# Kernel optimization log

Measured on AMD Instinct MI355X. Metric: run time of the kernel, lower is better.

## Reference

```python
import jax, jax.numpy as jnp
import numpy as np

N_NODES = 100000
LAYER_NUM = 3


def gcn_conv(x, src, dst, W, b, n):
    # PyG GCNConv: add self-loops, symmetric normalization D^-1/2 (A+I) D^-1/2, x@W, +b
    h = x @ W                                   # [N, out]
    ones = jnp.ones(src.shape[0], dtype=h.dtype)
    deg = jax.ops.segment_sum(ones, dst, num_segments=n) + 1.0  # +1 for self-loop
    dinv = jax.lax.rsqrt(deg)                   # deg >= 1 always (self-loop)
    norm = dinv[src] * dinv[dst]                # [E]
    msgs = h[src] * norm[:, None]               # gather + scale, [E, out]
    agg = jax.ops.segment_sum(msgs, dst, num_segments=n)
    agg = agg + h * (dinv * dinv)[:, None]      # self-loop contribution
    return agg + b


def setup_inputs() -> dict:
    key = jax.random.key(0)
    ks = jax.random.split(key, 8)
    in_d, mid_d, out_d = 512, 256, 40
    n, e = N_NODES, 1600000
    x = jax.random.normal(ks[0], (n, in_d), dtype=jnp.float32)
    edge_index = jax.random.randint(ks[1], (2, e), 0, n, dtype=jnp.int64)
    def glorot(k, fan_in, fan_out):
        s = jnp.sqrt(6.0 / (fan_in + fan_out))
        return jax.random.uniform(k, (fan_in, fan_out), jnp.float32, -s, s)
    W1 = glorot(ks[2], in_d, mid_d)
    b1 = jnp.zeros((mid_d,), jnp.float32)
    Wi = glorot(ks[3], mid_d, mid_d)
    bi = jnp.zeros((mid_d,), jnp.float32)
    W2 = glorot(ks[4], mid_d, out_d)
    b2 = jnp.zeros((out_d,), jnp.float32)
    return {"x": x, "edge_index": edge_index, "W1": W1, "b1": b1,
            "Wi": Wi, "bi": bi, "W2": W2, "b2": b2}


def reference(x, edge_index, W1, b1, Wi, bi, W2, b2):
    n = x.shape[0]
    src, dst = edge_index[0], edge_index[1]
    h = gcn_conv(x, src, dst, W1, b1, n)
    for _ in range(LAYER_NUM):
        h = gcn_conv(h, src, dst, Wi, bi, n)
        h = jax.nn.relu(h)
    emb = h  # detached embedding in original
    h = jax.nn.relu(h)
    h = gcn_conv(h, src, dst, W2, b2, n)
    return (jax.nn.log_softmax(h, axis=1), emb)
```

## Files before the change

kernel.cpp:

```cpp
#include <hip/hip_runtime.h>
#include <cmath>

typedef __attribute__((ext_vector_type(8))) short short8v;
typedef __attribute__((ext_vector_type(4))) short short4v;
typedef __attribute__((ext_vector_type(4))) float f32x4;

__device__ inline short f2bf(float f) {
  union { float f; unsigned u; } a; a.f = f;
  unsigned r = a.u + 0x7FFF + ((a.u >> 16) & 1);
  return (short)(r >> 16);
}
__device__ inline float bf2f(short b) {
  union { unsigned u; float f; } a; a.u = ((unsigned)(unsigned short)b) << 16;
  return a.f;
}

__global__ void count_deg_kernel(const int* __restrict__ dst, int* __restrict__ deg, int e) {
  int i = blockIdx.x * blockDim.x + threadIdx.x;
  int stride = gridDim.x * blockDim.x;
  for (; i < e; i += stride) atomicAdd(&deg[dst[i]], 1);
}

__global__ void dinv_kernel(const int* __restrict__ deg, float* __restrict__ dinv, int n) {
  int i = blockIdx.x * blockDim.x + threadIdx.x;
  if (i < n) dinv[i] = rsqrtf((float)deg[i] + 1.0f);
}

#define SCAN_T 1024
__global__ void scan_blocks_kernel(const int* __restrict__ deg, int* __restrict__ rs,
                                   int* __restrict__ bsum, int n) {
  __shared__ int s[SCAN_T];
  int t = threadIdx.x;
  int i = blockIdx.x * SCAN_T + t;
  int own = (i < n) ? deg[i] : 0;
  s[t] = own;
  for (int off = 1; off < SCAN_T; off <<= 1) {
    __syncthreads();
    int add = (t >= off) ? s[t - off] : 0;
    __syncthreads();
    s[t] += add;
  }
  if (i < n) rs[i] = s[t] - own;
  if (t == SCAN_T - 1) bsum[blockIdx.x] = s[t];
}

__global__ void scan_bsum_kernel(int* __restrict__ bsum, int nb) {
  __shared__ int s[128];
  int t = threadIdx.x;
  int v = (t < nb) ? bsum[t] : 0;
  s[t] = v;
  for (int off = 1; off < 128; off <<= 1) {
    __syncthreads();
    int add = (t >= off) ? s[t - off] : 0;
    __syncthreads();
    s[t] += add;
  }
  if (t < nb) bsum[t] = s[t] - v;
}

__global__ void add_off_kernel(int* __restrict__ rs, const int* __restrict__ bsum, int n) {
  int i = blockIdx.x * blockDim.x + threadIdx.x;
  if (i < n) rs[i] += bsum[i >> 10];
}

__global__ void fill_csr_kernel(const int* __restrict__ src, const int* __restrict__ dst,
                                const int* __restrict__ rs, int* __restrict__ cursor,
                                int* __restrict__ col, int e) {
  int i = blockIdx.x * blockDim.x + threadIdx.x;
  int stride = gridDim.x * blockDim.x;
  for (; i < e; i += stride) {
    int d = dst[i];
    int p = rs[d] + atomicAdd(&cursor[d], 1);
    col[p] = src[i];
  }
}

__global__ void convert_wt_kernel(const float* __restrict__ W, short* __restrict__ Wt,
                                  int K, int N) {
  int i = blockIdx.x * blockDim.x + threadIdx.x;
  if (i < K * N) {
    int k = i / N, nn = i - k * N;
    Wt[nn * K + k] = f2bf(W[i]);
  }
}

__global__ void convert_w2t_kernel(const float* __restrict__ W2, short* __restrict__ W2t) {
  int i = blockIdx.x * blockDim.x + threadIdx.x;
  if (i < 64 * 256) {
    int c = i >> 8, k = i & 255;
    W2t[i] = (c < 40) ? f2bf(W2[k * 40 + c]) : (short)0;
  }
}

template <int K, bool AF32>
__global__ __launch_bounds__(256, 2) void gemm_mfma_kernel(
    const void* __restrict__ Aptr, const short* __restrict__ Wt,
    const float* __restrict__ dinv, char* __restrict__ G8,
    float* __restrict__ gscale, int n) {
  __shared__ short As[64 * 64];
  __shared__ short Bs[256 * 64];
  __shared__ float rmax[4][64];
  int tid = threadIdx.x;
  int lane = tid & 63, wn = tid >> 6;
  int l15 = lane & 15, lh = lane >> 4;
  int rowBase = blockIdx.x * 64;

  f32x4 acc[4][4];
#pragma unroll
  for (int mi = 0; mi < 4; mi++)
#pragma unroll
    for (int ni = 0; ni < 4; ni++) acc[mi][ni] = (f32x4){0.f, 0.f, 0.f, 0.f};

  short8v aS[2], bS[8];

  auto LOAD = [&](int kt) {
#pragma unroll
    for (int i = 0; i < 2; i++) {
      int s = tid + i * 256;
      int r = s >> 3, u = s & 7;
      int gr = rowBase + r; if (gr >= n) gr = n - 1;
      if constexpr (AF32) {
        const float* ap = (const float*)Aptr + (size_t)gr * K + kt + u * 8;
        float4 f0 = *(const float4*)ap;
        float4 f1 = *(const float4*)(ap + 4);
        short8v v;
        v[0] = f2bf(f0.x); v[1] = f2bf(f0.y); v[2] = f2bf(f0.z); v[3] = f2bf(f0.w);
        v[4] = f2bf(f1.x); v[5] = f2bf(f1.y); v[6] = f2bf(f1.z); v[7] = f2bf(f1.w);
        aS[i] = v;
      } else {
        aS[i] = *(const short8v*)((const short*)Aptr + (size_t)gr * K + kt + u * 8);
      }
    }
#pragma unroll
    for (int i = 0; i < 8; i++) {
      int s = tid + i * 256;
      int r = s >> 3, u = s & 7;
      bS[i] = *(const short8v*)(Wt + (size_t)r * K + kt + u * 8);
    }
  };

  auto STORE = [&]() {
#pragma unroll
    for (int i = 0; i < 2; i++) {
      int s = tid + i * 256;
      int r = s >> 3, u = s & 7;
      *(short8v*)&As[r * 64 + ((u ^ (r & 7)) << 3)] = aS[i];
    }
#pragma unroll
    for (int i = 0; i < 8; i++) {
      int s = tid + i * 256;
      int r = s >> 3, u = s & 7;
      *(short8v*)&Bs[r * 64 + ((u ^ (r & 7)) << 3)] = bS[i];
    }
  };

  auto COMPUTE = [&]() {
#pragma unroll
    for (int kk = 0; kk < 2; kk++) {
      int u = kk * 4 + lh;
      short8v af[4], bf[4];
#pragma unroll
      for (int mi = 0; mi < 4; mi++) {
        int r = mi * 16 + l15;
        af[mi] = *(const short8v*)&As[r * 64 + ((u ^ (r & 7)) << 3)];
      }
#pragma unroll
      for (int ni = 0; ni < 4; ni++) {
        int r = wn * 64 + ni * 16 + l15;
        bf[ni] = *(const short8v*)&Bs[r * 64 + ((u ^ (r & 7)) << 3)];
      }
#pragma unroll
      for (int mi = 0; mi < 4; mi++)
#pragma unroll
        for (int ni = 0; ni < 4; ni++)
          acc[mi][ni] = __builtin_amdgcn_mfma_f32_16x16x32_bf16(
              af[mi], bf[ni], acc[mi][ni], 0, 0, 0);
    }
  };

  LOAD(0);
  STORE();
  __syncthreads();
  for (int kt = 64; kt < K; kt += 64) {
    LOAD(kt);
    COMPUTE();
    __syncthreads();
    STORE();
    __syncthreads();
  }
  COMPUTE();

#pragma unroll
  for (int mi = 0; mi < 4; mi++) {
#pragma unroll
    for (int j = 0; j < 4; j++) {
      float mx = 0.f;
#pragma unroll
      for (int ni = 0; ni < 4; ni++) mx = fmaxf(mx, fabsf(acc[mi][ni][j]));
      for (int off = 1; off < 16; off <<= 1)
        mx = fmaxf(mx, __shfl_xor(mx, off, 64));
      if (l15 == 0) rmax[wn][mi * 16 + lh * 4 + j] = mx;
    }
  }
  __syncthreads();
#pragma unroll
  for (int mi = 0; mi < 4; mi++) {
#pragma unroll
    for (int j = 0; j < 4; j++) {
      int r = mi * 16 + lh * 4 + j;
      int gr = rowBase + r;
      if (gr < n) {
        float cmax = fmaxf(fmaxf(rmax[0][r], rmax[1][r]),
                           fmaxf(rmax[2][r], rmax[3][r]));
        float inv = (cmax > 0.f) ? 127.f / cmax : 0.f;
        if (wn == 0 && l15 == 0)
          gscale[gr] = dinv[gr] * cmax * (1.f / 127.f);
#pragma unroll
        for (int ni = 0; ni < 4; ni++) {
          int gc = wn * 64 + ni * 16 + l15;
          int q = (int)rintf(acc[mi][ni][j] * inv);
          G8[(size_t)gr * 256 + gc] = (char)q;
        }
      }
    }
  }
}

__global__ __launch_bounds__(256, 3) void gemm_mfma40_kernel(
    const short* __restrict__ Hb, const short* __restrict__ W2t,
    const float* __restrict__ dinv, short* __restrict__ G2b, int n) {
  __shared__ short As[256 * 64];
  __shared__ short Bs[64 * 64];
  int tid = threadIdx.x;
  int lane = tid & 63, wid = tid >> 6;
  int l15 = lane & 15, lh = lane >> 4;
  int rowBase = blockIdx.x * 256;

  f32x4 acc[4][4];
#pragma unroll
  for (int mi = 0; mi < 4; mi++)
#pragma unroll
    for (int ni = 0; ni < 4; ni++) acc[mi][ni] = (f32x4){0.f, 0.f, 0.f, 0.f};

  for (int kt = 0; kt < 256; kt += 64) {
#pragma unroll
    for (int i = 0; i < 8; i++) {
      int s = tid + i * 256;
      int r = s >> 3, u = s & 7;
      int gr = rowBase + r; if (gr >= n) gr = n - 1;
      short8v v = *(const short8v*)(Hb + (size_t)gr * 256 + kt + u * 8);
      *(short8v*)&As[r * 64 + ((u ^ (r & 7)) << 3)] = v;
    }
#pragma unroll
    for (int i = 0; i < 2; i++) {
      int s = tid + i * 256;
      int r = s >> 3, u = s & 7;
      short8v v = *(const short8v*)(W2t + (size_t)r * 256 + kt + u * 8);
      *(short8v*)&Bs[r * 64 + ((u ^ (r & 7)) << 3)] = v;
    }
    __syncthreads();
#pragma unroll
    for (int kk = 0; kk < 2; kk++) {
      int u = kk * 4 + lh;
      short8v af[4], bf[4];
#pragma unroll
      for (int mi = 0; mi < 4; mi++) {
        int r = wid * 64 + mi * 16 + l15;
        af[mi] = *(const short8v*)&As[r * 64 + ((u ^ (r & 7)) << 3)];
      }
#pragma unroll
      for (int ni = 0; ni < 4; ni++) {
        int r = ni * 16 + l15;
        bf[ni] = *(const short8v*)&Bs[r * 64 + ((u ^ (r & 7)) << 3)];
      }
#pragma unroll
      for (int mi = 0; mi < 4; mi++)
#pragma unroll
        for (int ni = 0; ni < 4; ni++)
          acc[mi][ni] = __builtin_amdgcn_mfma_f32_16x16x32_bf16(
              af[mi], bf[ni], acc[mi][ni], 0, 0, 0);
    }
    __syncthreads();
  }

#pragma unroll
  for (int mi = 0; mi < 4; mi++) {
#pragma unroll
    for (int j = 0; j < 4; j++) {
      int gr = rowBase + wid * 64 + mi * 16 + lh * 4 + j;
      if (gr < n) {
        float sc = dinv[gr];
#pragma unroll
        for (int ni = 0; ni < 4; ni++) {
          int gc = ni * 16 + l15;
          if (gc < 40) G2b[(size_t)gr * 40 + gc] = f2bf(acc[mi][ni][j] * sc);
        }
      }
    }
  }
}

__device__ inline void dq_acc(int w, float s, float& a0, float& a1,
                              float& a2, float& a3) {
  a0 += (float)(signed char)(w & 0xff) * s;
  a1 += (float)(signed char)((w >> 8) & 0xff) * s;
  a2 += (float)(signed char)((w >> 16) & 0xff) * s;
  a3 += (float)(signed char)(w >> 24) * s;
}

template <int RELU, int WF32>
__global__ __launch_bounds__(256) void aggregate_i8_kernel(
    const char* __restrict__ G8, const float* __restrict__ gsc,
    const int* __restrict__ col, const int* __restrict__ rs,
    const int* __restrict__ deg, const float* __restrict__ dinv,
    const float* __restrict__ bias, short* __restrict__ Hb,
    float* __restrict__ Hf, int n) {
  int wid = threadIdx.x >> 6;
  int lane = threadIdx.x & 63;
  int v = blockIdx.x * 4 + wid;
  if (v >= n) return;
  float a0 = 0.f, a1 = 0.f, a2 = 0.f, a3 = 0.f;
  {
    int w = *(const int*)(G8 + (size_t)v * 256 + lane * 4);
    dq_acc(w, gsc[v], a0, a1, a2, a3);
  }
  int base = rs[v], cnt = deg[v];
  for (int i0 = 0; i0 < cnt; i0 += 64) {
    int rem = cnt - i0; if (rem > 64) rem = 64;
    int ci = col[base + i0 + (lane < rem ? lane : 0)];
    int i = 0;
    for (; i + 8 <= rem; i += 8) {
      int u0 = __shfl(ci, i + 0), u1 = __shfl(ci, i + 1);
      int u2 = __shfl(ci, i + 2), u3 = __shfl(ci, i + 3);
      int u4 = __shfl(ci, i + 4), u5 = __shfl(ci, i + 5);
      int u6 = __shfl(ci, i + 6), u7 = __shfl(ci, i + 7);
      int w0 = *(const int*)(G8 + (size_t)u0 * 256 + lane * 4);
      int w1 = *(const int*)(G8 + (size_t)u1 * 256 + lane * 4);
      int w2 = *(const int*)(G8 + (size_t)u2 * 256 + lane * 4);
      int w3 = *(const int*)(G8 + (size_t)u3 * 256 + lane * 4);
      int w4 = *(const int*)(G8 + (size_t)u4 * 256 + lane * 4);
      int w5 = *(const int*)(G8 + (size_t)u5 * 256 + lane * 4);
      int w6 = *(const int*)(G8 + (size_t)u6 * 256 + lane * 4);
      int w7 = *(const int*)(G8 + (size_t)u7 * 256 + lane * 4);
      float s0 = gsc[u0], s1 = gsc[u1], s2 = gsc[u2], s3 = gsc[u3];
      float s4 = gsc[u4], s5 = gsc[u5], s6 = gsc[u6], s7 = gsc[u7];
      dq_acc(w0, s0, a0, a1, a2, a3);
      dq_acc(w1, s1, a0, a1, a2, a3);
      dq_acc(w2, s2, a0, a1, a2, a3);
      dq_acc(w3, s3, a0, a1, a2, a3);
      dq_acc(w4, s4, a0, a1, a2, a3);
      dq_acc(w5, s5, a0, a1, a2, a3);
      dq_acc(w6, s6, a0, a1, a2, a3);
      dq_acc(w7, s7, a0, a1, a2, a3);
    }
    for (; i < rem; i++) {
      int u = __shfl(ci, i);
      int w = *(const int*)(G8 + (size_t)u * 256 + lane * 4);
      dq_acc(w, gsc[u], a0, a1, a2, a3);
    }
  }
  float s = dinv[v];
  float4 b4 = ((const float4*)bias)[lane];
  float o0 = a0 * s + b4.x, o1 = a1 * s + b4.y, o2 = a2 * s + b4.z, o3 = a3 * s + b4.w;
  if (RELU) {
    o0 = fmaxf(o0, 0.f); o1 = fmaxf(o1, 0.f);
    o2 = fmaxf(o2, 0.f); o3 = fmaxf(o3, 0.f);
  }
  short4v ob; ob[0] = f2bf(o0); ob[1] = f2bf(o1); ob[2] = f2bf(o2); ob[3] = f2bf(o3);
  *(short4v*)(Hb + (size_t)v * 256 + lane * 4) = ob;
  if (WF32) {
    float4 of; of.x = o0; of.y = o1; of.z = o2; of.w = o3;
    *(float4*)(Hf + (size_t)v * 256 + lane * 4) = of;
  }
}

__global__ __launch_bounds__(256) void agg40_lsm_kernel(
    const short* __restrict__ G2b, const int* __restrict__ col,
    const int* __restrict__ rs, const int* __restrict__ deg,
    const float* __restrict__ dinv, const float* __restrict__ b2,
    float* __restrict__ out, int n) {
  int wid = threadIdx.x >> 6;
  int lane = threadIdx.x & 63;
  int v = blockIdx.x * 4 + wid;
  if (v >= n) return;
  bool act = lane < 40;
  int ln = act ? lane : 0;
  float acc = act ? bf2f(G2b[(size_t)v * 40 + lane]) : 0.f;
  int base = rs[v], cnt = deg[v];
  for (int i0 = 0; i0 < cnt; i0 += 64) {
    int rem = cnt - i0; if (rem > 64) rem = 64;
    int ci = col[base + i0 + (lane < rem ? lane : 0)];
    int i = 0;
    for (; i + 4 <= rem; i += 4) {
      int u0 = __shfl(ci, i + 0), u1 = __shfl(ci, i + 1);
      int u2 = __shfl(ci, i + 2), u3 = __shfl(ci, i + 3);
      float x0 = bf2f(G2b[(size_t)u0 * 40 + ln]);
      float x1 = bf2f(G2b[(size_t)u1 * 40 + ln]);
      float x2 = bf2f(G2b[(size_t)u2 * 40 + ln]);
      float x3 = bf2f(G2b[(size_t)u3 * 40 + ln]);
      acc += x0 + x1 + x2 + x3;
    }
    for (; i < rem; i++) {
      int u = __shfl(ci, i);
      acc += bf2f(G2b[(size_t)u * 40 + ln]);
    }
  }
  float val;
  if (act) val = acc * dinv[v] + b2[lane];
  else val = -INFINITY;
  float m = val;
  for (int off = 32; off; off >>= 1) m = fmaxf(m, __shfl_xor(m, off, 64));
  float e = act ? expf(val - m) : 0.f;
  float ssum = e;
  for (int off = 32; off; off >>= 1) ssum += __shfl_xor(ssum, off, 64);
  if (act) out[(size_t)v * 40 + lane] = val - m - logf(ssum);
}


static inline size_t alignup(size_t x) { return (x + 255) & ~(size_t)255; }

extern "C" void kernel_launch(void* const* d_in, const int* in_sizes, int n_in,
                              void* d_out, int out_size, void* d_ws, size_t ws_size,
                              hipStream_t stream) {
  const float* x  = (const float*)d_in[0];
  const int*   ei = (const int*)d_in[1];
  const float* W1 = (const float*)d_in[2];
  const float* b1 = (const float*)d_in[3];
  const float* Wi = (const float*)d_in[4];
  const float* bi = (const float*)d_in[5];
  const float* W2 = (const float*)d_in[6];
  const float* b2 = (const float*)d_in[7];

  const int in_d = 512, mid_d = 256, out_d = 40;
  int n = in_sizes[0] / in_d;
  int E = in_sizes[1] / 2;
  const int* src = ei;
  const int* dst = ei + E;

  float* out_lsm = (float*)d_out;
  float* emb     = (float*)d_out + (size_t)n * out_d;

  char* w = (char*)d_ws;
  float* dinv  = (float*)w;  w += alignup((size_t)n * 4);
  int* deg     = (int*)w;    w += alignup((size_t)n * 4);
  int* rs      = (int*)w;    w += alignup((size_t)n * 4);
  int* cursor  = (int*)w;    w += alignup((size_t)n * 4);
  int* colidx  = (int*)w;    w += alignup((size_t)E * 4);
  int* bsum    = (int*)w;    w += alignup(128 * 4);
  short* W1t   = (short*)w;  w += alignup((size_t)mid_d * in_d * 2);
  short* Wit   = (short*)w;  w += alignup((size_t)mid_d * mid_d * 2);
  short* W2t   = (short*)w;  w += alignup((size_t)64 * mid_d * 2);
  char* G8     = (char*)w;   w += alignup((size_t)n * mid_d);
  float* gsc   = (float*)w;  w += alignup((size_t)n * 4);
  short* Hb    = (short*)w;  w += alignup((size_t)n * mid_d * 2);
  short* G2b   = (short*)G8;

  int nb = (n + SCAN_T - 1) / SCAN_T;

  hipMemsetAsync(deg, 0, (size_t)n * 4, stream);
  hipMemsetAsync(cursor, 0, (size_t)n * 4, stream);
  count_deg_kernel<<<2048, 256, 0, stream>>>(dst, deg, E);
  dinv_kernel<<<(n + 255) / 256, 256, 0, stream>>>(deg, dinv, n);
  scan_blocks_kernel<<<nb, SCAN_T, 0, stream>>>(deg, rs, bsum, n);
  scan_bsum_kernel<<<1, 128, 0, stream>>>(bsum, nb);
  add_off_kernel<<<(n + 255) / 256, 256, 0, stream>>>(rs, bsum, n);
  fill_csr_kernel<<<2048, 256, 0, stream>>>(src, dst, rs, cursor, colidx, E);

  convert_wt_kernel<<<(in_d * mid_d + 255) / 256, 256, 0, stream>>>(W1, W1t, in_d, mid_d);
  convert_wt_kernel<<<(mid_d * mid_d + 255) / 256, 256, 0, stream>>>(Wi, Wit, mid_d, mid_d);
  convert_w2t_kernel<<<(64 * mid_d + 255) / 256, 256, 0, stream>>>(W2, W2t);

  int ggrid = (n + 63) / 64;
  int agg_grid = (n + 3) / 4;

  gemm_mfma_kernel<512, true><<<ggrid, 256, 0, stream>>>(x, W1t, dinv, G8, gsc, n);
  aggregate_i8_kernel<0, 0><<<agg_grid, 256, 0, stream>>>(
      G8, gsc, colidx, rs, deg, dinv, b1, Hb, nullptr, n);
  for (int l = 0; l < 2; l++) {
    gemm_mfma_kernel<256, false><<<ggrid, 256, 0, stream>>>(Hb, Wit, dinv, G8, gsc, n);
    aggregate_i8_kernel<1, 0><<<agg_grid, 256, 0, stream>>>(
        G8, gsc, colidx, rs, deg, dinv, bi, Hb, nullptr, n);
  }
  gemm_mfma_kernel<256, false><<<ggrid, 256, 0, stream>>>(Hb, Wit, dinv, G8, gsc, n);
  aggregate_i8_kernel<1, 1><<<agg_grid, 256, 0, stream>>>(
      G8, gsc, colidx, rs, deg, dinv, bi, Hb, emb, n);

  gemm_mfma40_kernel<<<(n + 255) / 256, 256, 0, stream>>>(Hb, W2t, dinv, G2b, n);
  agg40_lsm_kernel<<<agg_grid, 256, 0, stream>>>(G2b, colidx, rs, deg, dinv, b2, out_lsm, n);
}
```

Baseline: 775.6 us.

## Build CSR via two-level bucketing of edges by destination block

```diff
diff --git a/kernel.cpp b/kernel.cpp
--- a/kernel.cpp
+++ b/kernel.cpp
@@ -15,63 +15,76 @@
   return a.f;
 }
 
-__global__ void count_deg_kernel(const int* __restrict__ dst, int* __restrict__ deg, int e) {
-  int i = blockIdx.x * blockDim.x + threadIdx.x;
-  int stride = gridDim.x * blockDim.x;
-  for (; i < e; i += stride) atomicAdd(&deg[dst[i]], 1);
-}
-
-__global__ void dinv_kernel(const int* __restrict__ deg, float* __restrict__ dinv, int n) {
-  int i = blockIdx.x * blockDim.x + threadIdx.x;
-  if (i < n) dinv[i] = rsqrtf((float)deg[i] + 1.0f);
-}
-
-#define SCAN_T 1024
-__global__ void scan_blocks_kernel(const int* __restrict__ deg, int* __restrict__ rs,
-                                   int* __restrict__ bsum, int n) {
-  __shared__ int s[SCAN_T];
-  int t = threadIdx.x;
-  int i = blockIdx.x * SCAN_T + t;
-  int own = (i < n) ? deg[i] : 0;
-  s[t] = own;
-  for (int off = 1; off < SCAN_T; off <<= 1) {
-    __syncthreads();
-    int add = (t >= off) ? s[t - off] : 0;
-    __syncthreads();
-    s[t] += add;
-  }
-  if (i < n) rs[i] = s[t] - own;
-  if (t == SCAN_T - 1) bsum[blockIdx.x] = s[t];
-}
-
-__global__ void scan_bsum_kernel(int* __restrict__ bsum, int nb) {
-  __shared__ int s[128];
-  int t = threadIdx.x;
-  int v = (t < nb) ? bsum[t] : 0;
-  s[t] = v;
-  for (int off = 1; off < 128; off <<= 1) {
-    __syncthreads();
-    int add = (t >= off) ? s[t - off] : 0;
-    __syncthreads();
-    s[t] += add;
-  }
-  if (t < nb) bsum[t] = s[t] - v;
-}
-
-__global__ void add_off_kernel(int* __restrict__ rs, const int* __restrict__ bsum, int n) {
-  int i = blockIdx.x * blockDim.x + threadIdx.x;
-  if (i < n) rs[i] += bsum[i >> 10];
-}
-
-__global__ void fill_csr_kernel(const int* __restrict__ src, const int* __restrict__ dst,
-                                const int* __restrict__ rs, int* __restrict__ cursor,
-                                int* __restrict__ col, int e) {
+__global__ void bin_edges_kernel(const int* __restrict__ src, const int* __restrict__ dst,
+                                 int* __restrict__ bktCur, uint2* __restrict__ pairBuf,
+                                 int e, int cap) {
   int i = blockIdx.x * blockDim.x + threadIdx.x;
   int stride = gridDim.x * blockDim.x;
   for (; i < e; i += stride) {
-    int d = dst[i];
-    int p = rs[d] + atomicAdd(&cursor[d], 1);
-    col[p] = src[i];
+    int d = dst[i], s = src[i];
+    int b = d >> 8;
+    int p = atomicAdd(&bktCur[b], 1);
+    pairBuf[(size_t)b * cap + p] = make_uint2((unsigned)d, (unsigned)s);
+  }
+}
+
+__global__ void scan_bkt_kernel(const int* __restrict__ bktCur, int* __restrict__ bktOff,
+                                int nb) {
+  __shared__ int s[512];
+  int t = threadIdx.x;
+  int v = (t < nb) ? bktCur[t] : 0;
+  s[t] = v;
+  for (int off = 1; off < 512; off <<= 1) {
+    __syncthreads();
+    int add = (t >= off) ? s[t - off] : 0;
+    __syncthreads();
+    s[t] += add;
+  }
+  if (t < nb) bktOff[t] = s[t] - v;
+}
+
+__global__ __launch_bounds__(256) void bucket_csr_kernel(
+    const uint2* __restrict__ pairBuf, const int* __restrict__ bktCur,
+    const int* __restrict__ bktOff, int* __restrict__ deg, int* __restrict__ rs,
+    float* __restrict__ dinv, int* __restrict__ col, int n, int cap) {
+  __shared__ int hist[256];
+  __shared__ int loff[256];
+  __shared__ int cur[256];
+  int b = blockIdx.x;
+  int base = b << 8;
+  int m = n - base; if (m > 256) m = 256;
+  int t = threadIdx.x;
+  hist[t] = 0;
+  __syncthreads();
+  int cnt = bktCur[b];
+  const uint2* pb = pairBuf + (size_t)b * cap;
+  for (int j = t; j < cnt; j += 256)
+    atomicAdd(&hist[pb[j].x - base], 1);
+  __syncthreads();
+  int own = hist[t];
+  loff[t] = own;
+  for (int off = 1; off < 256; off <<= 1) {
+    __syncthreads();
+    int add = (t >= off) ? loff[t - off] : 0;
+    __syncthreads();
+    loff[t] += add;
+  }
+  __syncthreads();
+  int excl = loff[t] - own;
+  int bo = bktOff[b];
+  if (t < m) {
+    deg[base + t] = own;
+    rs[base + t] = bo + excl;
+    dinv[base + t] = rsqrtf((float)own + 1.0f);
+  }
+  __syncthreads();
+  hist[t] = excl;
+  cur[t] = 0;
+  __syncthreads();
+  for (int j = t; j < cnt; j += 256) {
+    int d = pb[j].x - base;
+    int q = atomicAdd(&cur[d], 1);
+    col[bo + hist[d] + q] = (int)pb[j].y;
   }
 }
 
@@ -440,13 +453,17 @@
   float* out_lsm = (float*)d_out;
   float* emb     = (float*)d_out + (size_t)n * out_d;
 
+  int NB = (n + 255) >> 8;
+  int cap = ((E / NB) * 3) / 2 + 1024;
+
   char* w = (char*)d_ws;
   float* dinv  = (float*)w;  w += alignup((size_t)n * 4);
   int* deg     = (int*)w;    w += alignup((size_t)n * 4);
   int* rs      = (int*)w;    w += alignup((size_t)n * 4);
-  int* cursor  = (int*)w;    w += alignup((size_t)n * 4);
   int* colidx  = (int*)w;    w += alignup((size_t)E * 4);
-  int* bsum    = (int*)w;    w += alignup(128 * 4);
+  int* bktCur  = (int*)w;    w += alignup((size_t)NB * 4);
+  int* bktOff  = (int*)w;    w += alignup((size_t)NB * 4);
+  uint2* pairBuf = (uint2*)w; w += alignup((size_t)NB * cap * 8);
   short* W1t   = (short*)w;  w += alignup((size_t)mid_d * in_d * 2);
   short* Wit   = (short*)w;  w += alignup((size_t)mid_d * mid_d * 2);
   short* W2t   = (short*)w;  w += alignup((size_t)64 * mid_d * 2);
@@ -455,16 +472,11 @@
   short* Hb    = (short*)w;  w += alignup((size_t)n * mid_d * 2);
   short* G2b   = (short*)G8;
 
-  int nb = (n + SCAN_T - 1) / SCAN_T;
-
-  hipMemsetAsync(deg, 0, (size_t)n * 4, stream);
-  hipMemsetAsync(cursor, 0, (size_t)n * 4, stream);
-  count_deg_kernel<<<2048, 256, 0, stream>>>(dst, deg, E);
-  dinv_kernel<<<(n + 255) / 256, 256, 0, stream>>>(deg, dinv, n);
-  scan_blocks_kernel<<<nb, SCAN_T, 0, stream>>>(deg, rs, bsum, n);
-  scan_bsum_kernel<<<1, 128, 0, stream>>>(bsum, nb);
-  add_off_kernel<<<(n + 255) / 256, 256, 0, stream>>>(rs, bsum, n);
-  fill_csr_kernel<<<2048, 256, 0, stream>>>(src, dst, rs, cursor, colidx, E);
+  hipMemsetAsync(bktCur, 0, (size_t)NB * 4, stream);
+  bin_edges_kernel<<<2048, 256, 0, stream>>>(src, dst, bktCur, pairBuf, E, cap);
+  scan_bkt_kernel<<<1, 512, 0, stream>>>(bktCur, bktOff, NB);
+  bucket_csr_kernel<<<NB, 256, 0, stream>>>(pairBuf, bktCur, bktOff,
+                                            deg, rs, dinv, colidx, n, cap);
 
   convert_wt_kernel<<<(in_d * mid_d + 255) / 256, 256, 0, stream>>>(W1, W1t, in_d, mid_d);
   convert_wt_kernel<<<(mid_d * mid_d + 255) / 256, 256, 0, stream>>>(Wi, Wit, mid_d, mid_d);
```

Result: slower. 1.194 ms (+53.9%).
